# Kernel optimization log

Hardware: AMD Instinct MI355X
Metric: run time of the kernel (lower is better)

## Reference

```python
import jax, jax.numpy as jnp
import numpy as np

NUM_USER = 10000
NUM_ITEM = 30000
N = NUM_USER + NUM_ITEM          # total nodes
DIM = 64                          # dim_E == dim_C
E = 500000                        # user-item interactions
NUM_ROUTING = 3
ALPHA_THR = 0.5
NEG_SLOPE_ATTN = 0.2              # GAT attention leaky slope
NEG_SLOPE_ACT = 0.01              # F.leaky_relu_ default


def l2norm(x, eps=1e-12):
    n = jnp.linalg.norm(x, axis=-1, keepdims=True)
    return x / jnp.maximum(n, eps)


def seg_softmax(score, seg):
    # numerically-stable softmax over edges grouped by destination node
    m = jax.ops.segment_max(score, seg, num_segments=N)
    e = jnp.exp(score - m[seg])
    s = jax.ops.segment_sum(e, seg, num_segments=N)
    return e / (s[seg] + 1e-16)


def gat_ori(x, W, src, dst):
    # GATConv_ori: dot-product attention, softmax per destination, scatter-add
    h = x @ W                                     # [N, C]
    score = jax.nn.leaky_relu(jnp.sum(h[dst] * h[src], -1), NEG_SLOPE_ATTN)
    alpha = seg_softmax(score, dst)               # [2E]
    return jax.ops.segment_sum(alpha[:, None] * h[src], dst, num_segments=N)


def gat_pre(x, y, z, W, src, dst):
    # GATConv_pre: primary-modality attention modulated by cross-modal gate (reattn)
    hx = x @ W
    sx = jnp.sum(hx[dst] * hx[src], -1)
    sy = jnp.sum(y[dst] * y[src], -1)
    sz = jnp.sum(z[dst] * z[src], -1)
    alpha = seg_softmax(jax.nn.leaky_relu(sx, NEG_SLOPE_ATTN), dst)
    gate = jax.nn.sigmoid(0.5 * (sy + sz))
    alpha = jnp.where(gate > ALPHA_THR, alpha * gate, alpha)
    return jax.ops.segment_sum(alpha[:, None] * hx[src], dst, num_segments=N)


def cgcn(pref, feat, pref2, feat2, pref3, feat3, src, dst, Wpre, Wori):
    x = jnp.concatenate([pref, feat], 0)
    y = jnp.concatenate([pref2, feat2], 0)
    z = jnp.concatenate([pref3, feat3], 0)
    x = l2norm(gat_pre(x, y, z, Wpre, src, dst))
    for _ in range(NUM_ROUTING):
        x = l2norm(x + gat_ori(x, Wori, src, dst))
    return x


def gcn_conv(x, W, src, dst):
    return jax.ops.segment_sum((x @ W)[src], dst, num_segments=N)


def real_gcn(id_emb, Wg, src, dst):
    x = l2norm(id_emb)
    h1 = jax.nn.leaky_relu(gcn_conv(x, Wg[0], src, dst), NEG_SLOPE_ACT)
    h2 = jax.nn.leaky_relu(gcn_conv(h1, Wg[1], src, dst), NEG_SLOPE_ACT)
    h3 = gcn_conv(h1, Wg[2], src, dst)
    return x + h1 + h2 + h3


def setup_inputs() -> dict:
    key = jax.random.key(0)
    ks = jax.random.split(key, 16)
    users = jax.random.randint(ks[0], (E,), 0, NUM_USER)
    items = jax.random.randint(ks[1], (E,), NUM_USER, N)
    edge_index = jnp.stack([users, items]).astype(jnp.int64)
    s = 0.05
    return {
        'edge_index': edge_index,
        'v_feat': jax.random.normal(ks[2], (NUM_ITEM, 128), jnp.float32),
        'a_feat': jax.random.normal(ks[3], (NUM_ITEM, 128), jnp.float32),
        't_feat': jax.random.normal(ks[4], (NUM_ITEM, 100), jnp.float32),
        'pref_v': jax.random.normal(ks[5], (NUM_USER, DIM), jnp.float32) * s,
        'pref_a': jax.random.normal(ks[6], (NUM_USER, DIM), jnp.float32) * s,
        'pref_t': jax.random.normal(ks[7], (NUM_USER, DIM), jnp.float32) * s,
        'mlp_v_w': jax.random.normal(ks[8], (DIM, 128), jnp.float32) * s,
        'mlp_v_b': jnp.zeros((DIM,), jnp.float32),
        'mlp_a_w': jax.random.normal(ks[9], (DIM, 128), jnp.float32) * s,
        'mlp_a_b': jnp.zeros((DIM,), jnp.float32),
        'mlp_t_w': jax.random.normal(ks[10], (DIM, 100), jnp.float32) * s,
        'mlp_t_b': jnp.zeros((DIM,), jnp.float32),
        'pre_w': jax.random.normal(ks[11], (3, DIM, DIM), jnp.float32) * s,
        'ori_w': jax.random.normal(ks[12], (3, DIM, DIM), jnp.float32) * s,
        'gcn_w': jax.random.normal(ks[13], (3, DIM, DIM), jnp.float32) * s,
        'id_embedding': jax.random.normal(ks[14], (N, DIM), jnp.float32) * s,
    }


def reference(edge_index, v_feat, a_feat, t_feat, pref_v, pref_a, pref_t,
              mlp_v_w, mlp_v_b, mlp_a_w, mlp_a_b, mlp_t_w, mlp_t_b,
              pre_w, ori_w, gcn_w, id_embedding):
    # symmetrize edges (cat with flipped); no self-loops possible (bipartite)
    src = jnp.concatenate([edge_index[0], edge_index[1]])
    dst = jnp.concatenate([edge_index[1], edge_index[0]])

    fv = l2norm(jax.nn.leaky_relu(v_feat @ mlp_v_w.T + mlp_v_b, NEG_SLOPE_ACT))
    fa = l2norm(jax.nn.leaky_relu(a_feat @ mlp_a_w.T + mlp_a_b, NEG_SLOPE_ACT))
    ft = l2norm(jax.nn.leaky_relu(t_feat @ mlp_t_w.T + mlp_t_b, NEG_SLOPE_ACT))
    pv, pa, pt = l2norm(pref_v), l2norm(pref_a), l2norm(pref_t)

    v_rep = cgcn(pv, fv, pa, fa, pt, ft, src, dst, pre_w[0], ori_w[0])
    a_rep = cgcn(pa, fa, pv, fv, pt, ft, src, dst, pre_w[1], ori_w[1])
    t_rep = cgcn(pt, ft, pa, fa, pv, fv, src, dst, pre_w[2], ori_w[2])
    id_rep = real_gcn(id_embedding, gcn_w, src, dst)

    return jnp.concatenate([id_rep, v_rep, a_rep, t_rep], axis=1)  # [N, 4*DIM]
```

## Files before the change

### kernel.cpp

```cpp
#include <hip/hip_runtime.h>
#include <hip/hip_fp16.h>
#include <math.h>

#define NUSER 10000
#define NITEM 30000
#define NN    40000
#define DD    64
#define PLANE ((size_t)NN * DD)

typedef _Float16 hv2 __attribute__((ext_vector_type(2)));
typedef _Float16 half8v __attribute__((ext_vector_type(8)));
typedef float float4v __attribute__((ext_vector_type(4)));
union U2H { unsigned u; hv2 v; __half2 hh; };

#if defined(__has_builtin)
#if __has_builtin(__builtin_amdgcn_fdot2)
#define HAS_FDOT2 1
#endif
#endif

__device__ __forceinline__ float fdot2u(unsigned a, unsigned b, float c) {
#ifdef HAS_FDOT2
    U2H x, y;
    x.u = a;
    y.u = b;
    return __builtin_amdgcn_fdot2(x.v, y.v, c, false);
#else
    U2H x, y;
    x.u = a;
    y.u = b;
    float2 fa = __half22float2(x.hh), fb = __half22float2(y.hh);
    return c + fa.x * fb.x + fa.y * fb.y;
#endif
}

__device__ __forceinline__ float dot8(uint4 a, uint4 b) {
    float d = fdot2u(a.x, b.x, 0.f);
    d = fdot2u(a.y, b.y, d);
    d = fdot2u(a.z, b.z, d);
    d = fdot2u(a.w, b.w, d);
    return d;
}

__device__ __forceinline__ __half2 uh(unsigned u) { U2H x; x.u = u; return x.hh; }
__device__ __forceinline__ unsigned hu(__half2 h) { U2H x; x.hh = h; return x.u; }
__device__ __forceinline__ __half2 h2rx(__half2 v, int m) {
    return __hadd2(v, uh((unsigned)__shfl_xor((int)hu(v), m, 64)));
}

__device__ __forceinline__ float wsum(float v) {
#pragma unroll
    for (int o = 32; o > 0; o >>= 1) v += __shfl_xor(v, o, 64);
    return v;
}
__device__ __forceinline__ float qsum8(float v) {
    v += __shfl_xor(v, 1, 64);
    v += __shfl_xor(v, 2, 64);
    v += __shfl_xor(v, 4, 64);
    return v;
}
__device__ __forceinline__ float gsum8f(float v) {
    v += __shfl_xor(v, 8, 64);
    v += __shfl_xor(v, 16, 64);
    v += __shfl_xor(v, 32, 64);
    return v;
}

__device__ __forceinline__ int orderIF(int i) {
    return (i < NITEM) ? (NUSER + i) : (i - NITEM);
}

__global__ void k_hist(const int* ei, int E2, int E, int* cnt, int* posw) {
    int i = blockIdx.x * blockDim.x + threadIdx.x;
    if (i >= E2) return;
    int d = (i < E) ? ei[E + i] : ei[i - E];
    posw[i] = atomicAdd(&cnt[d], 1);
}

__global__ void k_bsum(const int* __restrict__ cnt, int* __restrict__ bsum, int n, int chunk) {
    __shared__ int wsh[4];
    int b = blockIdx.x, tid = threadIdx.x;
    int base = b * chunk, end = min(n, base + chunk);
    int s = 0;
    for (int i = base + tid; i < end; i += 256) s += cnt[i];
#pragma unroll
    for (int o = 32; o > 0; o >>= 1) s += __shfl_xor(s, o, 64);
    if ((tid & 63) == 0) wsh[tid >> 6] = s;
    __syncthreads();
    if (tid == 0) bsum[b] = wsh[0] + wsh[1] + wsh[2] + wsh[3];
}

__global__ void k_bscan(int* bsum, int nb, int* rp_end) {
    int lane = threadIdx.x;
    int v = (lane < nb) ? bsum[lane] : 0;
    int orig = v;
#pragma unroll
    for (int o = 1; o < 64; o <<= 1) {
        int y = __shfl_up(v, o, 64);
        if (lane >= o) v += y;
    }
    if (lane < nb) bsum[lane] = v - orig;
    if (lane == 63) *rp_end = v;
}

__global__ void k_apply(const int* __restrict__ cnt, const int* __restrict__ boff,
                        int* __restrict__ rp, int n, int chunk) {
    __shared__ int buf[256];
    __shared__ int csh;
    int b = blockIdx.x, tid = threadIdx.x;
    int base = b * chunk, end = min(n, base + chunk);
    int carry = boff[b];
    for (int t0 = base; t0 < end; t0 += 256) {
        int i = t0 + tid;
        int v = (i < end) ? cnt[i] : 0;
        int x = v;
        buf[tid] = x;
        __syncthreads();
        for (int o = 1; o < 256; o <<= 1) {
            int y = (tid >= o) ? buf[tid - o] : 0;
            __syncthreads();
            x += y;
            buf[tid] = x;
            __syncthreads();
        }
        if (i < end) rp[i] = carry + x - v;
        __syncthreads();
        if (tid == 255) csh = carry + x;
        __syncthreads();
        carry = csh;
    }
}

__global__ void k_scatter(const int* ei, int E2, int E, const int* rp,
                          const int* __restrict__ posw, int* col) {
    int i = blockIdx.x * blockDim.x + threadIdx.x;
    if (i >= E2) return;
    int j = (i < E) ? i : i - E;
    int s = (i < E) ? ei[j] : ei[E + j];
    int d = (i < E) ? ei[E + j] : ei[j];
    col[rp[d] + posw[i]] = s;
}

__global__ void k_prep_pref(const float* __restrict__ pv, const float* __restrict__ pa,
                            const float* __restrict__ pt, __half* __restrict__ M) {
    int t = blockIdx.x * blockDim.x + threadIdx.x;
    int w = t >> 6, lane = t & 63, nw = (gridDim.x * blockDim.x) >> 6;
    for (int r = w; r < NUSER; r += nw) {
        float a = pv[(size_t)r * DD + lane];
        float b = pa[(size_t)r * DD + lane];
        float c = pt[(size_t)r * DD + lane];
        float sa = a * a, sb = b * b, sc = c * c;
#pragma unroll
        for (int o = 32; o > 0; o >>= 1) {
            sa += __shfl_xor(sa, o, 64);
            sb += __shfl_xor(sb, o, 64);
            sc += __shfl_xor(sc, o, 64);
        }
        size_t base = (size_t)r * 3 * DD + lane;
        M[base] = __float2half(a / fmaxf(sqrtf(sa), 1e-12f));
        M[base + DD] = __float2half(b / fmaxf(sqrtf(sb), 1e-12f));
        M[base + 2 * DD] = __float2half(c / fmaxf(sqrtf(sc), 1e-12f));
    }
}

template <int K>
__global__ void k_mlp(const float* __restrict__ feat, const float* __restrict__ W,
                      const float* __restrict__ bias, __half* __restrict__ M, int mo) {
    constexpr int K4 = K / 4;
    __shared__ float4 Wl[K4][DD];
    __shared__ float4 rbuf[4][2][K4];
    int t = threadIdx.x, wib = t >> 6, lane = t & 63;
    for (int i = t; i < DD * K4; i += 256) {
        int c = i / K4, k4 = i - c * K4;
        Wl[k4][c] = *(const float4*)(W + (size_t)c * K + k4 * 4);
    }
    __syncthreads();
    float b = bias[lane];
    const int stride = gridDim.x * 4;
    int r = blockIdx.x * 4 + wib;
    float4 v = {0.f, 0.f, 0.f, 0.f};
    if (r < NITEM && lane < K4) v = *(const float4*)(feat + (size_t)r * K + lane * 4);
    int cur = 0;
    for (; r < NITEM; r += stride) {
        if (lane < K4) rbuf[wib][cur][lane] = v;
        int rn = r + stride;
        if (rn < NITEM && lane < K4) v = *(const float4*)(feat + (size_t)rn * K + lane * 4);
        asm volatile("s_waitcnt lgkmcnt(0)" ::: "memory");
        float acc = b;
#pragma unroll
        for (int k4 = 0; k4 < K4; k4++) {
            float4 x4 = rbuf[wib][cur][k4];
            float4 w4 = Wl[k4][lane];
            acc += x4.x * w4.x + x4.y * w4.y + x4.z * w4.z + x4.w * w4.w;
        }
        float h = acc > 0.f ? acc : 0.01f * acc;
        float n = sqrtf(wsum(h * h));
        M[((size_t)(NUSER + r) * 3 + mo) * DD + lane] = __float2half(h / fmaxf(n, 1e-12f));
        cur ^= 1;
    }
}

__global__ void k_gemm_mfma(const __half* __restrict__ x3, const float* __restrict__ W3,
                            __half* __restrict__ o3) {
    int mo = blockIdx.y;
    const float* W = W3 + (size_t)mo * 4096;
    int t = threadIdx.x, wv = t >> 6, lane = t & 63;
    int lr = lane & 15, lg = lane >> 4;
    half8v b[4][2];
#pragma unroll
    for (int ct = 0; ct < 4; ct++)
#pragma unroll
        for (int kh = 0; kh < 2; kh++)
#pragma unroll
            for (int i = 0; i < 8; i++)
                b[ct][kh][i] = (_Float16)W[(kh * 32 + lg * 8 + i) * 64 + ct * 16 + lr];
    const int NT = NN / 16;
    for (int rt = blockIdx.x * 4 + wv; rt < NT; rt += gridDim.x * 4) {
        const __half* xr = x3 + ((size_t)(rt * 16 + lr) * 3 + mo) * DD + lg * 8;
        half8v a0 = *(const half8v*)xr;
        half8v a1 = *(const half8v*)(xr + 32);
        float4v acc0 = {0.f, 0.f, 0.f, 0.f}, acc1 = acc0, acc2 = acc0, acc3 = acc0;
        acc0 = __builtin_amdgcn_mfma_f32_16x16x32_f16(a0, b[0][0], acc0, 0, 0, 0);
        acc1 = __builtin_amdgcn_mfma_f32_16x16x32_f16(a0, b[1][0], acc1, 0, 0, 0);
        acc2 = __builtin_amdgcn_mfma_f32_16x16x32_f16(a0, b[2][0], acc2, 0, 0, 0);
        acc3 = __builtin_amdgcn_mfma_f32_16x16x32_f16(a0, b[3][0], acc3, 0, 0, 0);
        acc0 = __builtin_amdgcn_mfma_f32_16x16x32_f16(a1, b[0][1], acc0, 0, 0, 0);
        acc1 = __builtin_amdgcn_mfma_f32_16x16x32_f16(a1, b[1][1], acc1, 0, 0, 0);
        acc2 = __builtin_amdgcn_mfma_f32_16x16x32_f16(a1, b[2][1], acc2, 0, 0, 0);
        acc3 = __builtin_amdgcn_mfma_f32_16x16x32_f16(a1, b[3][1], acc3, 0, 0, 0);
#pragma unroll
        for (int i = 0; i < 4; i++) {
            size_t rbase = ((size_t)(rt * 16 + lg * 4 + i) * 3 + mo) * DD + lr;
            o3[rbase] = __float2half(acc0[i]);
            o3[rbase + 16] = __float2half(acc1[i]);
            o3[rbase + 32] = __float2half(acc2[i]);
            o3[rbase + 48] = __float2half(acc3[i]);
        }
    }
}

__global__ void k_gemm_f2(const float* __restrict__ x, const float* __restrict__ W2,
                          __half* __restrict__ o2) {
    __shared__ float rowbuf[4][DD];
    int mo = blockIdx.y;
    const float* W = W2 + (size_t)mo * 4096;
    int t = threadIdx.x, wib = t >> 6, lane = t & 63;
    float Wc[DD];
#pragma unroll
    for (int k = 0; k < DD; k++) Wc[k] = W[k * DD + lane];
    for (int r = blockIdx.x * 4 + wib; r < NN; r += gridDim.x * 4) {
        rowbuf[wib][lane] = x[(size_t)r * DD + lane];
        asm volatile("s_waitcnt lgkmcnt(0)" ::: "memory");
        float acc = 0.f;
#pragma unroll
        for (int k4 = 0; k4 < DD / 4; k4++) {
            float4 xq = *(const float4*)&rowbuf[wib][k4 * 4];
            acc += xq.x * Wc[k4 * 4] + xq.y * Wc[k4 * 4 + 1] + xq.z * Wc[k4 * 4 + 2] +
                   xq.w * Wc[k4 * 4 + 3];
        }
        o2[((size_t)r * 2 + mo) * DD + lane] = __float2half(acc);
    }
}

__global__ void k_gemm_id(const float* __restrict__ x, const float* __restrict__ W,
                          __half* __restrict__ hout, float* __restrict__ xnorm) {
    __shared__ float rowbuf[4][DD];
    int t = threadIdx.x, wib = t >> 6, lane = t & 63;
    float Wc[DD];
#pragma unroll
    for (int k = 0; k < DD; k++) Wc[k] = W[k * DD + lane];
    for (int r = blockIdx.x * 4 + wib; r < NN; r += gridDim.x * 4) {
        float xv = x[(size_t)r * DD + lane];
        float n = sqrtf(wsum(xv * xv));
        xv /= fmaxf(n, 1e-12f);
        xnorm[(size_t)r * DD + lane] = xv;
        rowbuf[wib][lane] = xv;
        asm volatile("s_waitcnt lgkmcnt(0)" ::: "memory");
        float acc = 0.f;
#pragma unroll
        for (int k4 = 0; k4 < DD / 4; k4++) {
            float4 xq = *(const float4*)&rowbuf[wib][k4 * 4];
            acc += xq.x * Wc[k4 * 4] + xq.y * Wc[k4 * 4 + 1] + xq.z * Wc[k4 * 4 + 2] +
                   xq.w * Wc[k4 * 4 + 3];
        }
        hout[(size_t)r * DD + lane] = __float2half(acc);
    }
}

__device__ __forceinline__ float gatef(float ssum) {
    float gate = 1.f / (1.f + __expf(-0.5f * ssum));
    return gate > 0.5f ? gate : 1.f;
}

__global__ void k_gat_pre3(const __half* __restrict__ M, const __half* __restrict__ h3,
                           const int* __restrict__ rp, const int* __restrict__ col,
                           __half* __restrict__ x3h) {
    int t = blockIdx.x * blockDim.x + threadIdx.x;
    int wv = t >> 6, lane = t & 63, nw = (gridDim.x * blockDim.x) >> 6;
    int g = lane >> 3, q = lane & 7;
    const __half2 z = __floats2half2_rn(0.f, 0.f);
    for (int w0 = wv; w0 < NN; w0 += nw) {
        int n = orderIF(w0);
        int e0 = rp[n], e1 = rp[n + 1];
        const uint4* mrow = (const uint4*)(M + (size_t)n * 192);
        uint4 tv = mrow[q], ta = mrow[q + 8], tt = mrow[q + 16];
        const uint4* hrow = (const uint4*)(h3 + (size_t)n * 192);
        uint4 hd0 = hrow[q], hd1 = hrow[q + 8], hd2 = hrow[q + 16];
        float s0 = 0.f, s1 = 0.f, s2 = 0.f;
        __half2 a0[4] = {z, z, z, z}, a1[4] = {z, z, z, z}, a2[4] = {z, z, z, z};
        for (int eb = e0 + g; eb < e1; eb += 8) {
            int sn = col[eb];
            const uint4* srow = (const uint4*)(M + (size_t)sn * 192);
            uint4 sv = srow[q], sa = srow[q + 8], st = srow[q + 16];
            float dv = qsum8(dot8(tv, sv));
            float da = qsum8(dot8(ta, sa));
            float dt = qsum8(dot8(tt, st));
            float ga = gatef(da + dt), gb_ = gatef(dv + dt), gc = gatef(da + dv);
            const uint4* hsrow = (const uint4*)(h3 + (size_t)sn * 192);
            uint4 v0 = hsrow[q], v1 = hsrow[q + 8], v2 = hsrow[q + 16];
            float d0 = qsum8(dot8(hd0, v0));
            float d1 = qsum8(dot8(hd1, v1));
            float d2 = qsum8(dot8(hd2, v2));
            float sc0 = d0 > 0.f ? d0 : 0.2f * d0;
            float sc1 = d1 > 0.f ? d1 : 0.2f * d1;
            float sc2 = d2 > 0.f ? d2 : 0.2f * d2;
            float p0 = __expf(sc0), p1 = __expf(sc1), p2 = __expf(sc2);
            s0 += p0;
            s1 += p1;
            s2 += p2;
            __half2 ph0 = __float2half2_rn(p0 * ga);
            __half2 ph1 = __float2half2_rn(p1 * gb_);
            __half2 ph2 = __float2half2_rn(p2 * gc);
            a0[0] = __hfma2(ph0, uh(v0.x), a0[0]);
            a0[1] = __hfma2(ph0, uh(v0.y), a0[1]);
            a0[2] = __hfma2(ph0, uh(v0.z), a0[2]);
            a0[3] = __hfma2(ph0, uh(v0.w), a0[3]);
            a1[0] = __hfma2(ph1, uh(v1.x), a1[0]);
            a1[1] = __hfma2(ph1, uh(v1.y), a1[1]);
            a1[2] = __hfma2(ph1, uh(v1.z), a1[2]);
            a1[3] = __hfma2(ph1, uh(v1.w), a1[3]);
            a2[0] = __hfma2(ph2, uh(v2.x), a2[0]);
            a2[1] = __hfma2(ph2, uh(v2.y), a2[1]);
            a2[2] = __hfma2(ph2, uh(v2.z), a2[2]);
            a2[3] = __hfma2(ph2, uh(v2.w), a2[3]);
        }
        s0 = gsum8f(s0);
        s1 = gsum8f(s1);
        s2 = gsum8f(s2);
#pragma unroll
        for (int j = 0; j < 4; j++) {
            a0[j] = h2rx(h2rx(h2rx(a0[j], 8), 16), 32);
            a1[j] = h2rx(h2rx(h2rx(a1[j], 8), 16), 32);
            a2[j] = h2rx(h2rx(h2rx(a2[j], 8), 16), 32);
        }
        float i0 = 1.f / (s0 + 1e-16f), i1 = 1.f / (s1 + 1e-16f), i2 = 1.f / (s2 + 1e-16f);
        float o0[8], o1[8], o2[8];
#pragma unroll
        for (int j = 0; j < 4; j++) {
            float2 f0 = __half22float2(a0[j]);
            float2 f1 = __half22float2(a1[j]);
            float2 f2 = __half22float2(a2[j]);
            o0[2 * j] = f0.x * i0;
            o0[2 * j + 1] = f0.y * i0;
            o1[2 * j] = f1.x * i1;
            o1[2 * j + 1] = f1.y * i1;
            o2[2 * j] = f2.x * i2;
            o2[2 * j + 1] = f2.y * i2;
        }
        float n0 = 0.f, n1 = 0.f, n2 = 0.f;
#pragma unroll
        for (int k = 0; k < 8; k++) {
            n0 += o0[k] * o0[k];
            n1 += o1[k] * o1[k];
            n2 += o2[k] * o2[k];
        }
        n0 = qsum8(n0);
        n1 = qsum8(n1);
        n2 = qsum8(n2);
        float r0 = 1.f / fmaxf(sqrtf(n0), 1e-12f);
        float r1 = 1.f / fmaxf(sqrtf(n1), 1e-12f);
        float r2 = 1.f / fmaxf(sqrtf(n2), 1e-12f);
        if (g == 0) {
            uint4* orow = (uint4*)(x3h + (size_t)n * 192);
            uint4 w0_, w1_, w2_;
            w0_.x = hu(__floats2half2_rn(o0[0] * r0, o0[1] * r0));
            w0_.y = hu(__floats2half2_rn(o0[2] * r0, o0[3] * r0));
            w0_.z = hu(__floats2half2_rn(o0[4] * r0, o0[5] * r0));
            w0_.w = hu(__floats2half2_rn(o0[6] * r0, o0[7] * r0));
            w1_.x = hu(__floats2half2_rn(o1[0] * r1, o1[1] * r1));
            w1_.y = hu(__floats2half2_rn(o1[2] * r1, o1[3] * r1));
            w1_.z = hu(__floats2half2_rn(o1[4] * r1, o1[5] * r1));
            w1_.w = hu(__floats2half2_rn(o1[6] * r1, o1[7] * r1));
            w2_.x = hu(__floats2half2_rn(o2[0] * r2, o2[1] * r2));
            w2_.y = hu(__floats2half2_rn(o2[2] * r2, o2[3] * r2));
            w2_.z = hu(__floats2half2_rn(o2[4] * r2, o2[5] * r2));
            w2_.w = hu(__floats2half2_rn(o2[6] * r2, o2[7] * r2));
            orow[q] = w0_;
            orow[q + 8] = w1_;
            orow[q + 16] = w2_;
        }
    }
}

__global__ void k_gat_ori3(const __half* __restrict__ h3, const __half* __restrict__ x3h,
                           const int* __restrict__ rp, const int* __restrict__ col,
                           __half* __restrict__ xout, float* __restrict__ fout) {
    int t = blockIdx.x * blockDim.x + threadIdx.x;
    int wv = t >> 6, lane = t & 63, nw = (gridDim.x * blockDim.x) >> 6;
    int g = lane >> 3, q = lane & 7;
    const __half2 z = __floats2half2_rn(0.f, 0.f);
    for (int w0 = wv; w0 < NN; w0 += nw) {
        int n = orderIF(w0);
        int e0 = rp[n], e1 = rp[n + 1];
        const uint4* hrow = (const uint4*)(h3 + (size_t)n * 192);
        uint4 hd0 = hrow[q], hd1 = hrow[q + 8], hd2 = hrow[q + 16];
        float s0 = 0.f, s1 = 0.f, s2 = 0.f;
        __half2 a0[4] = {z, z, z, z}, a1[4] = {z, z, z, z}, a2[4] = {z, z, z, z};
        for (int eb = e0 + g; eb < e1; eb += 8) {
            int sn = col[eb];
            const uint4* srow = (const uint4*)(h3 + (size_t)sn * 192);
            uint4 v0 = srow[q], v1 = srow[q + 8], v2 = srow[q + 16];
            float d0 = qsum8(dot8(hd0, v0));
            float d1 = qsum8(dot8(hd1, v1));
            float d2 = qsum8(dot8(hd2, v2));
            float sc0 = d0 > 0.f ? d0 : 0.2f * d0;
            float sc1 = d1 > 0.f ? d1 : 0.2f * d1;
            float sc2 = d2 > 0.f ? d2 : 0.2f * d2;
            float p0 = __expf(sc0), p1 = __expf(sc1), p2 = __expf(sc2);
            s0 += p0;
            s1 += p1;
            s2 += p2;
            __half2 ph0 = __float2half2_rn(p0);
            __half2 ph1 = __float2half2_rn(p1);
            __half2 ph2 = __float2half2_rn(p2);
            a0[0] = __hfma2(ph0, uh(v0.x), a0[0]);
            a0[1] = __hfma2(ph0, uh(v0.y), a0[1]);
            a0[2] = __hfma2(ph0, uh(v0.z), a0[2]);
            a0[3] = __hfma2(ph0, uh(v0.w), a0[3]);
            a1[0] = __hfma2(ph1, uh(v1.x), a1[0]);
            a1[1] = __hfma2(ph1, uh(v1.y), a1[1]);
            a1[2] = __hfma2(ph1, uh(v1.z), a1[2]);
            a1[3] = __hfma2(ph1, uh(v1.w), a1[3]);
            a2[0] = __hfma2(ph2, uh(v2.x), a2[0]);
            a2[1] = __hfma2(ph2, uh(v2.y), a2[1]);
            a2[2] = __hfma2(ph2, uh(v2.z), a2[2]);
            a2[3] = __hfma2(ph2, uh(v2.w), a2[3]);
        }
        s0 = gsum8f(s0);
        s1 = gsum8f(s1);
        s2 = gsum8f(s2);
#pragma unroll
        for (int j = 0; j < 4; j++) {
            a0[j] = h2rx(h2rx(h2rx(a0[j], 8), 16), 32);
            a1[j] = h2rx(h2rx(h2rx(a1[j], 8), 16), 32);
            a2[j] = h2rx(h2rx(h2rx(a2[j], 8), 16), 32);
        }
        float i0 = 1.f / (s0 + 1e-16f), i1 = 1.f / (s1 + 1e-16f), i2 = 1.f / (s2 + 1e-16f);
        const uint4* xrow = (const uint4*)(x3h + (size_t)n * 192);
        uint4 xr0 = xrow[q], xr1 = xrow[q + 8], xr2 = xrow[q + 16];
        float o0[8], o1[8], o2[8];
#pragma unroll
        for (int j = 0; j < 4; j++) {
            float2 f0 = __half22float2(a0[j]);
            float2 f1 = __half22float2(a1[j]);
            float2 f2 = __half22float2(a2[j]);
            float2 xf0 = __half22float2(uh(j == 0 ? xr0.x : j == 1 ? xr0.y : j == 2 ? xr0.z : xr0.w));
            float2 xf1 = __half22float2(uh(j == 0 ? xr1.x : j == 1 ? xr1.y : j == 2 ? xr1.z : xr1.w));
            float2 xf2 = __half22float2(uh(j == 0 ? xr2.x : j == 1 ? xr2.y : j == 2 ? xr2.z : xr2.w));
            o0[2 * j] = xf0.x + f0.x * i0;
            o0[2 * j + 1] = xf0.y + f0.y * i0;
            o1[2 * j] = xf1.x + f1.x * i1;
            o1[2 * j + 1] = xf1.y + f1.y * i1;
            o2[2 * j] = xf2.x + f2.x * i2;
            o2[2 * j + 1] = xf2.y + f2.y * i2;
        }
        float n0 = 0.f, n1 = 0.f, n2 = 0.f;
#pragma unroll
        for (int k = 0; k < 8; k++) {
            n0 += o0[k] * o0[k];
            n1 += o1[k] * o1[k];
            n2 += o2[k] * o2[k];
        }
        n0 = qsum8(n0);
        n1 = qsum8(n1);
        n2 = qsum8(n2);
        float r0 = 1.f / fmaxf(sqrtf(n0), 1e-12f);
        float r1 = 1.f / fmaxf(sqrtf(n1), 1e-12f);
        float r2 = 1.f / fmaxf(sqrtf(n2), 1e-12f);
        if (g == 0) {
            if (fout) {
                float* ob = fout + (size_t)n * 256 + 64 + q * 8;
                *(float4*)(ob) = make_float4(o0[0] * r0, o0[1] * r0, o0[2] * r0, o0[3] * r0);
                *(float4*)(ob + 4) = make_float4(o0[4] * r0, o0[5] * r0, o0[6] * r0, o0[7] * r0);
                *(float4*)(ob + 64) = make_float4(o1[0] * r1, o1[1] * r1, o1[2] * r1, o1[3] * r1);
                *(float4*)(ob + 68) = make_float4(o1[4] * r1, o1[5] * r1, o1[6] * r1, o1[7] * r1);
                *(float4*)(ob + 128) = make_float4(o2[0] * r2, o2[1] * r2, o2[2] * r2, o2[3] * r2);
                *(float4*)(ob + 132) = make_float4(o2[4] * r2, o2[5] * r2, o2[6] * r2, o2[7] * r2);
            } else {
                uint4* orow = (uint4*)(xout + (size_t)n * 192);
                uint4 w0_, w1_, w2_;
                w0_.x = hu(__floats2half2_rn(o0[0] * r0, o0[1] * r0));
                w0_.y = hu(__floats2half2_rn(o0[2] * r0, o0[3] * r0));
                w0_.z = hu(__floats2half2_rn(o0[4] * r0, o0[5] * r0));
                w0_.w = hu(__floats2half2_rn(o0[6] * r0, o0[7] * r0));
                w1_.x = hu(__floats2half2_rn(o1[0] * r1, o1[1] * r1));
                w1_.y = hu(__floats2half2_rn(o1[2] * r1, o1[3] * r1));
                w1_.z = hu(__floats2half2_rn(o1[4] * r1, o1[5] * r1));
                w1_.w = hu(__floats2half2_rn(o1[6] * r1, o1[7] * r1));
                w2_.x = hu(__floats2half2_rn(o2[0] * r2, o2[1] * r2));
                w2_.y = hu(__floats2half2_rn(o2[2] * r2, o2[3] * r2));
                w2_.z = hu(__floats2half2_rn(o2[4] * r2, o2[5] * r2));
                w2_.w = hu(__floats2half2_rn(o2[6] * r2, o2[7] * r2));
                orow[q] = w0_;
                orow[q + 8] = w1_;
                orow[q + 16] = w2_;
            }
        }
    }
}

__global__ void k_gcn1(const __half* __restrict__ h, const int* __restrict__ rp,
                       const int* __restrict__ col, float* __restrict__ out) {
    int t = blockIdx.x * blockDim.x + threadIdx.x;
    int wv = t >> 6, lane = t & 63, nw = (gridDim.x * blockDim.x) >> 6;
    int g = lane >> 3, q = lane & 7;
    const __half2 z = __floats2half2_rn(0.f, 0.f);
    for (int w0 = wv; w0 < NN; w0 += nw) {
        int n = orderIF(w0);
        int e0 = rp[n], e1 = rp[n + 1];
        __half2 a[4] = {z, z, z, z};
        for (int eb = e0 + g; eb < e1; eb += 8) {
            int sn = col[eb];
            uint4 v = ((const uint4*)(h + (size_t)sn * DD))[q];
            a[0] = __hadd2(a[0], uh(v.x));
            a[1] = __hadd2(a[1], uh(v.y));
            a[2] = __hadd2(a[2], uh(v.z));
            a[3] = __hadd2(a[3], uh(v.w));
        }
#pragma unroll
        for (int j = 0; j < 4; j++) a[j] = h2rx(h2rx(h2rx(a[j], 8), 16), 32);
        if (g == 0) {
            float o[8];
#pragma unroll
            for (int j = 0; j < 4; j++) {
                float2 f = __half22float2(a[j]);
                o[2 * j] = f.x > 0.f ? f.x : 0.01f * f.x;
                o[2 * j + 1] = f.y > 0.f ? f.y : 0.01f * f.y;
            }
            float* ob = out + (size_t)n * DD + q * 8;
            *(float4*)(ob) = make_float4(o[0], o[1], o[2], o[3]);
            *(float4*)(ob + 4) = make_float4(o[4], o[5], o[6], o[7]);
        }
    }
}

__global__ void k_gcn_final2(const __half* __restrict__ gp, const int* __restrict__ rp,
                             const int* __restrict__ col, const float* __restrict__ x0,
                             const float* __restrict__ h1, float* __restrict__ out) {
    int t = blockIdx.x * blockDim.x + threadIdx.x;
    int wv = t >> 6, lane = t & 63, nw = (gridDim.x * blockDim.x) >> 6;
    int g = lane >> 3, q = lane & 7;
    const __half2 z = __floats2half2_rn(0.f, 0.f);
    for (int w0 = wv; w0 < NN; w0 += nw) {
        int n = orderIF(w0);
        int e0 = rp[n], e1 = rp[n + 1];
        __half2 aA[4] = {z, z, z, z}, aB[4] = {z, z, z, z};
        for (int eb = e0 + g; eb < e1; eb += 8) {
            int sn = col[eb];
            const uint4* base = (const uint4*)(gp + (size_t)sn * 128);
            uint4 vA = base[q], vB = base[q + 8];
            aA[0] = __hadd2(aA[0], uh(vA.x));
            aA[1] = __hadd2(aA[1], uh(vA.y));
            aA[2] = __hadd2(aA[2], uh(vA.z));
            aA[3] = __hadd2(aA[3], uh(vA.w));
            aB[0] = __hadd2(aB[0], uh(vB.x));
            aB[1] = __hadd2(aB[1], uh(vB.y));
            aB[2] = __hadd2(aB[2], uh(vB.z));
            aB[3] = __hadd2(aB[3], uh(vB.w));
        }
#pragma unroll
        for (int j = 0; j < 4; j++) {
            aA[j] = h2rx(h2rx(h2rx(aA[j], 8), 16), 32);
            aB[j] = h2rx(h2rx(h2rx(aB[j], 8), 16), 32);
        }
        if (g == 0) {
            const float* p0 = x0 + (size_t)n * DD + q * 8;
            const float* p1 = h1 + (size_t)n * DD + q * 8;
            float4 v0a = *(const float4*)(p0), v0b = *(const float4*)(p0 + 4);
            float4 v1a = *(const float4*)(p1), v1b = *(const float4*)(p1 + 4);
            float o[8];
#pragma unroll
            for (int j = 0; j < 4; j++) {
                float2 fA = __half22float2(aA[j]);
                float2 fB = __half22float2(aB[j]);
                float h2x = fA.x > 0.f ? fA.x : 0.01f * fA.x;
                float h2y = fA.y > 0.f ? fA.y : 0.01f * fA.y;
                o[2 * j] = h2x + fB.x;
                o[2 * j + 1] = h2y + fB.y;
            }
            float* ob = out + (size_t)n * 256 + q * 8;
            *(float4*)(ob) = make_float4(o[0] + v0a.x + v1a.x, o[1] + v0a.y + v1a.y,
                                         o[2] + v0a.z + v1a.z, o[3] + v0a.w + v1a.w);
            *(float4*)(ob + 4) = make_float4(o[4] + v0b.x + v1b.x, o[5] + v0b.y + v1b.y,
                                             o[6] + v0b.z + v1b.z, o[7] + v0b.w + v1b.w);
        }
    }
}

extern "C" void kernel_launch(void* const* d_in, const int* in_sizes, int n_in,
                              void* d_out, int out_size, void* d_ws, size_t ws_size,
                              hipStream_t stream) {
    const int* ei       = (const int*)d_in[0];
    const float* v_feat = (const float*)d_in[1];
    const float* a_feat = (const float*)d_in[2];
    const float* t_feat = (const float*)d_in[3];
    const float* pref_v = (const float*)d_in[4];
    const float* pref_a = (const float*)d_in[5];
    const float* pref_t = (const float*)d_in[6];
    const float* mlp_v_w = (const float*)d_in[7];
    const float* mlp_v_b = (const float*)d_in[8];
    const float* mlp_a_w = (const float*)d_in[9];
    const float* mlp_a_b = (const float*)d_in[10];
    const float* mlp_t_w = (const float*)d_in[11];
    const float* mlp_t_b = (const float*)d_in[12];
    const float* pre_w  = (const float*)d_in[13];
    const float* ori_w  = (const float*)d_in[14];
    const float* gcn_w  = (const float*)d_in[15];
    const float* id_emb = (const float*)d_in[16];
    float* out = (float*)d_out;

    const int E2 = in_sizes[0];
    const int E  = E2 / 2;

    char* w = (char*)d_ws;
    auto alloc = [&](size_t bytes) -> void* {
        void* p = (void*)w;
        w += (bytes + 255) & ~(size_t)255;
        return p;
    };
    int* cnt  = (int*)alloc((size_t)NN * 4);
    int* rp   = (int*)alloc((size_t)(NN + 1) * 4);
    int* bsum = (int*)alloc(256);
    int* col  = (int*)alloc((size_t)E2 * 4);
    int* posw = (int*)alloc((size_t)E2 * 4);
    __half* Mh3  = (__half*)alloc(3 * PLANE * 2);
    __half* hb3h = (__half*)alloc(3 * PLANE * 2);
    __half* x3h  = (__half*)alloc(3 * PLANE * 2);
    float* x0f = (float*)alloc(PLANE * 4);
    float* h1f = (float*)alloc(PLANE * 4);

    __half* g1 = hb3h;
    __half* gpair = hb3h + PLANE;

    const int NBLK = 64, CHUNK = (NN + NBLK - 1) / NBLK;
    hipMemsetAsync(cnt, 0, (size_t)NN * 4, stream);
    k_hist<<<(E2 + 255) / 256, 256, 0, stream>>>(ei, E2, E, cnt, posw);
    k_bsum<<<NBLK, 256, 0, stream>>>(cnt, bsum, NN, CHUNK);
    k_bscan<<<1, 64, 0, stream>>>(bsum, NBLK, rp + NN);
    k_apply<<<NBLK, 256, 0, stream>>>(cnt, bsum, rp, NN, CHUNK);
    k_scatter<<<(E2 + 255) / 256, 256, 0, stream>>>(ei, E2, E, rp, posw, col);

    k_prep_pref<<<640, 256, 0, stream>>>(pref_v, pref_a, pref_t, Mh3);
    k_mlp<128><<<1024, 256, 0, stream>>>(v_feat, mlp_v_w, mlp_v_b, Mh3, 0);
    k_mlp<128><<<1024, 256, 0, stream>>>(a_feat, mlp_a_w, mlp_a_b, Mh3, 1);
    k_mlp<100><<<1024, 256, 0, stream>>>(t_feat, mlp_t_w, mlp_t_b, Mh3, 2);

    const int GB = (NN + 3) / 4;

    dim3 gm(640, 3);
    k_gemm_mfma<<<gm, 256, 0, stream>>>(Mh3, pre_w, hb3h);
    k_gat_pre3<<<GB, 256, 0, stream>>>(Mh3, hb3h, rp, col, x3h);
    for (int it = 0; it < 3; it++) {
        k_gemm_mfma<<<gm, 256, 0, stream>>>(x3h, ori_w, hb3h);
        if (it < 2)
            k_gat_ori3<<<GB, 256, 0, stream>>>(hb3h, x3h, rp, col, x3h, nullptr);
        else
            k_gat_ori3<<<GB, 256, 0, stream>>>(hb3h, x3h, rp, col, nullptr, out);
    }

    k_gemm_id<<<1280, 256, 0, stream>>>(id_emb, gcn_w, g1, x0f);
    k_gcn1<<<GB, 256, 0, stream>>>(g1, rp, col, h1f);
    dim3 g2(1280, 2);
    k_gemm_f2<<<g2, 256, 0, stream>>>(h1f, gcn_w + 4096, gpair);
    k_gcn_final2<<<GB, 256, 0, stream>>>(gpair, rp, col, x0f, h1f, out);
}
```

Baseline: 546.5 us.

## Fuse GCN neighbor aggregations into the GAT pre and final ori passes

The id-GCN branch's two edge-gather passes (k_gcn1 and k_gcn_final2) are folded into the existing GAT kernels. The first GCN aggregation now runs inside k_gat_pre3 and the second inside a new final-iteration k_gat_ori3f, so the CSR traversal and col reads are shared and two launches go away. To allow this, g1 and gpair get their own buffers instead of aliasing hb3h, and the GCN GEMMs are moved earlier in the schedule. The fused kernels carry more live registers and more gather traffic per edge, which may lower occupancy.

```diff
diff --git a/kernel.cpp b/kernel.cpp
--- a/kernel.cpp
+++ b/kernel.cpp
@@ -293,8 +293,9 @@
 }
 
 __global__ void k_gat_pre3(const __half* __restrict__ M, const __half* __restrict__ h3,
-                           const int* __restrict__ rp, const int* __restrict__ col,
-                           __half* __restrict__ x3h) {
+                           const __half* __restrict__ g1, const int* __restrict__ rp,
+                           const int* __restrict__ col, __half* __restrict__ x3h,
+                           float* __restrict__ h1f) {
     int t = blockIdx.x * blockDim.x + threadIdx.x;
     int wv = t >> 6, lane = t & 63, nw = (gridDim.x * blockDim.x) >> 6;
     int g = lane >> 3, q = lane & 7;
@@ -308,6 +309,7 @@
         uint4 hd0 = hrow[q], hd1 = hrow[q + 8], hd2 = hrow[q + 16];
         float s0 = 0.f, s1 = 0.f, s2 = 0.f;
         __half2 a0[4] = {z, z, z, z}, a1[4] = {z, z, z, z}, a2[4] = {z, z, z, z};
+        __half2 ag[4] = {z, z, z, z};
         for (int eb = e0 + g; eb < e1; eb += 8) {
             int sn = col[eb];
             const uint4* srow = (const uint4*)(M + (size_t)sn * 192);
@@ -318,6 +320,7 @@
             float ga = gatef(da + dt), gb_ = gatef(dv + dt), gc = gatef(da + dv);
             const uint4* hsrow = (const uint4*)(h3 + (size_t)sn * 192);
             uint4 v0 = hsrow[q], v1 = hsrow[q + 8], v2 = hsrow[q + 16];
+            uint4 vg = ((const uint4*)(g1 + (size_t)sn * DD))[q];
             float d0 = qsum8(dot8(hd0, v0));
             float d1 = qsum8(dot8(hd1, v1));
             float d2 = qsum8(dot8(hd2, v2));
@@ -343,6 +346,10 @@
             a2[1] = __hfma2(ph2, uh(v2.y), a2[1]);
             a2[2] = __hfma2(ph2, uh(v2.z), a2[2]);
             a2[3] = __hfma2(ph2, uh(v2.w), a2[3]);
+            ag[0] = __hadd2(ag[0], uh(vg.x));
+            ag[1] = __hadd2(ag[1], uh(vg.y));
+            ag[2] = __hadd2(ag[2], uh(vg.z));
+            ag[3] = __hadd2(ag[3], uh(vg.w));
         }
         s0 = gsum8f(s0);
         s1 = gsum8f(s1);
@@ -352,6 +359,7 @@
             a0[j] = h2rx(h2rx(h2rx(a0[j], 8), 16), 32);
             a1[j] = h2rx(h2rx(h2rx(a1[j], 8), 16), 32);
             a2[j] = h2rx(h2rx(h2rx(a2[j], 8), 16), 32);
+            ag[j] = h2rx(h2rx(h2rx(ag[j], 8), 16), 32);
         }
         float i0 = 1.f / (s0 + 1e-16f), i1 = 1.f / (s1 + 1e-16f), i2 = 1.f / (s2 + 1e-16f);
         float o0[8], o1[8], o2[8];
@@ -398,13 +406,23 @@
             orow[q] = w0_;
             orow[q + 8] = w1_;
             orow[q + 16] = w2_;
+            float og[8];
+#pragma unroll
+            for (int j = 0; j < 4; j++) {
+                float2 f = __half22float2(ag[j]);
+                og[2 * j] = f.x > 0.f ? f.x : 0.01f * f.x;
+                og[2 * j + 1] = f.y > 0.f ? f.y : 0.01f * f.y;
+            }
+            float* ob = h1f + (size_t)n * DD + q * 8;
+            *(float4*)(ob) = make_float4(og[0], og[1], og[2], og[3]);
+            *(float4*)(ob + 4) = make_float4(og[4], og[5], og[6], og[7]);
         }
     }
 }
 
 __global__ void k_gat_ori3(const __half* __restrict__ h3, const __half* __restrict__ x3h,
                            const int* __restrict__ rp, const int* __restrict__ col,
-                           __half* __restrict__ xout, float* __restrict__ fout) {
+                           __half* __restrict__ xout) {
     int t = blockIdx.x * blockDim.x + threadIdx.x;
     int wv = t >> 6, lane = t & 63, nw = (gridDim.x * blockDim.x) >> 6;
     int g = lane >> 3, q = lane & 7;
@@ -488,39 +506,31 @@
         float r1 = 1.f / fmaxf(sqrtf(n1), 1e-12f);
         float r2 = 1.f / fmaxf(sqrtf(n2), 1e-12f);
         if (g == 0) {
-            if (fout) {
-                float* ob = fout + (size_t)n * 256 + 64 + q * 8;
-                *(float4*)(ob) = make_float4(o0[0] * r0, o0[1] * r0, o0[2] * r0, o0[3] * r0);
-                *(float4*)(ob + 4) = make_float4(o0[4] * r0, o0[5] * r0, o0[6] * r0, o0[7] * r0);
-                *(float4*)(ob + 64) = make_float4(o1[0] * r1, o1[1] * r1, o1[2] * r1, o1[3] * r1);
-                *(float4*)(ob + 68) = make_float4(o1[4] * r1, o1[5] * r1, o1[6] * r1, o1[7] * r1);
-                *(float4*)(ob + 128) = make_float4(o2[0] * r2, o2[1] * r2, o2[2] * r2, o2[3] * r2);
-                *(float4*)(ob + 132) = make_float4(o2[4] * r2, o2[5] * r2, o2[6] * r2, o2[7] * r2);
-            } else {
-                uint4* orow = (uint4*)(xout + (size_t)n * 192);
-                uint4 w0_, w1_, w2_;
-                w0_.x = hu(__floats2half2_rn(o0[0] * r0, o0[1] * r0));
-                w0_.y = hu(__floats2half2_rn(o0[2] * r0, o0[3] * r0));
-                w0_.z = hu(__floats2half2_rn(o0[4] * r0, o0[5] * r0));
-                w0_.w = hu(__floats2half2_rn(o0[6] * r0, o0[7] * r0));
-                w1_.x = hu(__floats2half2_rn(o1[0] * r1, o1[1] * r1));
-                w1_.y = hu(__floats2half2_rn(o1[2] * r1, o1[3] * r1));
-                w1_.z = hu(__floats2half2_rn(o1[4] * r1, o1[5] * r1));
-                w1_.w = hu(__floats2half2_rn(o1[6] * r1, o1[7] * r1));
-                w2_.x = hu(__floats2half2_rn(o2[0] * r2, o2[1] * r2));
-                w2_.y = hu(__floats2half2_rn(o2[2] * r2, o2[3] * r2));
-                w2_.z = hu(__floats2half2_rn(o2[4] * r2, o2[5] * r2));
-                w2_.w = hu(__floats2half2_rn(o2[6] * r2, o2[7] * r2));
-                orow[q] = w0_;
-                orow[q + 8] = w1_;
-                orow[q + 16] = w2_;
-            }
-        }
-    }
-}
-
-__global__ void k_gcn1(const __half* __restrict__ h, const int* __restrict__ rp,
-                       const int* __restrict__ col, float* __restrict__ out) {
+            uint4* orow = (uint4*)(xout + (size_t)n * 192);
+            uint4 w0_, w1_, w2_;
+            w0_.x = hu(__floats2half2_rn(o0[0] * r0, o0[1] * r0));
+            w0_.y = hu(__floats2half2_rn(o0[2] * r0, o0[3] * r0));
+            w0_.z = hu(__floats2half2_rn(o0[4] * r0, o0[5] * r0));
+            w0_.w = hu(__floats2half2_rn(o0[6] * r0, o0[7] * r0));
+            w1_.x = hu(__floats2half2_rn(o1[0] * r1, o1[1] * r1));
+            w1_.y = hu(__floats2half2_rn(o1[2] * r1, o1[3] * r1));
+            w1_.z = hu(__floats2half2_rn(o1[4] * r1, o1[5] * r1));
+            w1_.w = hu(__floats2half2_rn(o1[6] * r1, o1[7] * r1));
+            w2_.x = hu(__floats2half2_rn(o2[0] * r2, o2[1] * r2));
+            w2_.y = hu(__floats2half2_rn(o2[2] * r2, o2[3] * r2));
+            w2_.z = hu(__floats2half2_rn(o2[4] * r2, o2[5] * r2));
+            w2_.w = hu(__floats2half2_rn(o2[6] * r2, o2[7] * r2));
+            orow[q] = w0_;
+            orow[q + 8] = w1_;
+            orow[q + 16] = w2_;
+        }
+    }
+}
+
+__global__ void k_gat_ori3f(const __half* __restrict__ h3, const __half* __restrict__ x3h,
+                            const __half* __restrict__ gp, const float* __restrict__ x0,
+                            const float* __restrict__ h1, const int* __restrict__ rp,
+                            const int* __restrict__ col, float* __restrict__ out) {
     int t = blockIdx.x * blockDim.x + threadIdx.x;
     int wv = t >> 6, lane = t & 63, nw = (gridDim.x * blockDim.x) >> 6;
     int g = lane >> 3, q = lane & 7;
@@ -528,47 +538,42 @@
     for (int w0 = wv; w0 < NN; w0 += nw) {
         int n = orderIF(w0);
         int e0 = rp[n], e1 = rp[n + 1];
-        __half2 a[4] = {z, z, z, z};
-        for (int eb = e0 + g; eb < e1; eb += 8) {
-            int sn = col[eb];
-            uint4 v = ((const uint4*)(h + (size_t)sn * DD))[q];
-            a[0] = __hadd2(a[0], uh(v.x));
-            a[1] = __hadd2(a[1], uh(v.y));
-            a[2] = __hadd2(a[2], uh(v.z));
-            a[3] = __hadd2(a[3], uh(v.w));
-        }
-#pragma unroll
-        for (int j = 0; j < 4; j++) a[j] = h2rx(h2rx(h2rx(a[j], 8), 16), 32);
-        if (g == 0) {
-            float o[8];
-#pragma unroll
-            for (int j = 0; j < 4; j++) {
-                float2 f = __half22float2(a[j]);
-                o[2 * j] = f.x > 0.f ? f.x : 0.01f * f.x;
-                o[2 * j + 1] = f.y > 0.f ? f.y : 0.01f * f.y;
-            }
-            float* ob = out + (size_t)n * DD + q * 8;
-            *(float4*)(ob) = make_float4(o[0], o[1], o[2], o[3]);
-            *(float4*)(ob + 4) = make_float4(o[4], o[5], o[6], o[7]);
-        }
-    }
-}
-
-__global__ void k_gcn_final2(const __half* __restrict__ gp, const int* __restrict__ rp,
-                             const int* __restrict__ col, const float* __restrict__ x0,
-                             const float* __restrict__ h1, float* __restrict__ out) {
-    int t = blockIdx.x * blockDim.x + threadIdx.x;
-    int wv = t >> 6, lane = t & 63, nw = (gridDim.x * blockDim.x) >> 6;
-    int g = lane >> 3, q = lane & 7;
-    const __half2 z = __floats2half2_rn(0.f, 0.f);
-    for (int w0 = wv; w0 < NN; w0 += nw) {
-        int n = orderIF(w0);
-        int e0 = rp[n], e1 = rp[n + 1];
+        const uint4* hrow = (const uint4*)(h3 + (size_t)n * 192);
+        uint4 hd0 = hrow[q], hd1 = hrow[q + 8], hd2 = hrow[q + 16];
+        float s0 = 0.f, s1 = 0.f, s2 = 0.f;
+        __half2 a0[4] = {z, z, z, z}, a1[4] = {z, z, z, z}, a2[4] = {z, z, z, z};
         __half2 aA[4] = {z, z, z, z}, aB[4] = {z, z, z, z};
         for (int eb = e0 + g; eb < e1; eb += 8) {
             int sn = col[eb];
-            const uint4* base = (const uint4*)(gp + (size_t)sn * 128);
-            uint4 vA = base[q], vB = base[q + 8];
+            const uint4* srow = (const uint4*)(h3 + (size_t)sn * 192);
+            uint4 v0 = srow[q], v1 = srow[q + 8], v2 = srow[q + 16];
+            const uint4* gbase = (const uint4*)(gp + (size_t)sn * 128);
+            uint4 vA = gbase[q], vB = gbase[q + 8];
+            float d0 = qsum8(dot8(hd0, v0));
+            float d1 = qsum8(dot8(hd1, v1));
+            float d2 = qsum8(dot8(hd2, v2));
+            float sc0 = d0 > 0.f ? d0 : 0.2f * d0;
+            float sc1 = d1 > 0.f ? d1 : 0.2f * d1;
+            float sc2 = d2 > 0.f ? d2 : 0.2f * d2;
+            float p0 = __expf(sc0), p1 = __expf(sc1), p2 = __expf(sc2);
+            s0 += p0;
+            s1 += p1;
+            s2 += p2;
+            __half2 ph0 = __float2half2_rn(p0);
+            __half2 ph1 = __float2half2_rn(p1);
+            __half2 ph2 = __float2half2_rn(p2);
+            a0[0] = __hfma2(ph0, uh(v0.x), a0[0]);
+            a0[1] = __hfma2(ph0, uh(v0.y), a0[1]);
+            a0[2] = __hfma2(ph0, uh(v0.z), a0[2]);
+            a0[3] = __hfma2(ph0, uh(v0.w), a0[3]);
+            a1[0] = __hfma2(ph1, uh(v1.x), a1[0]);
+            a1[1] = __hfma2(ph1, uh(v1.y), a1[1]);
+            a1[2] = __hfma2(ph1, uh(v1.z), a1[2]);
+            a1[3] = __hfma2(ph1, uh(v1.w), a1[3]);
+            a2[0] = __hfma2(ph2, uh(v2.x), a2[0]);
+            a2[1] = __hfma2(ph2, uh(v2.y), a2[1]);
+            a2[2] = __hfma2(ph2, uh(v2.z), a2[2]);
+            a2[3] = __hfma2(ph2, uh(v2.w), a2[3]);
             aA[0] = __hadd2(aA[0], uh(vA.x));
             aA[1] = __hadd2(aA[1], uh(vA.y));
             aA[2] = __hadd2(aA[2], uh(vA.z));
@@ -578,31 +583,75 @@
             aB[2] = __hadd2(aB[2], uh(vB.z));
             aB[3] = __hadd2(aB[3], uh(vB.w));
         }
+        s0 = gsum8f(s0);
+        s1 = gsum8f(s1);
+        s2 = gsum8f(s2);
 #pragma unroll
         for (int j = 0; j < 4; j++) {
+            a0[j] = h2rx(h2rx(h2rx(a0[j], 8), 16), 32);
+            a1[j] = h2rx(h2rx(h2rx(a1[j], 8), 16), 32);
+            a2[j] = h2rx(h2rx(h2rx(a2[j], 8), 16), 32);
             aA[j] = h2rx(h2rx(h2rx(aA[j], 8), 16), 32);
             aB[j] = h2rx(h2rx(h2rx(aB[j], 8), 16), 32);
         }
+        float i0 = 1.f / (s0 + 1e-16f), i1 = 1.f / (s1 + 1e-16f), i2 = 1.f / (s2 + 1e-16f);
+        const uint4* xrow = (const uint4*)(x3h + (size_t)n * 192);
+        uint4 xr0 = xrow[q], xr1 = xrow[q + 8], xr2 = xrow[q + 16];
+        float o0[8], o1[8], o2[8];
+#pragma unroll
+        for (int j = 0; j < 4; j++) {
+            float2 f0 = __half22float2(a0[j]);
+            float2 f1 = __half22float2(a1[j]);
+            float2 f2 = __half22float2(a2[j]);
+            float2 xf0 = __half22float2(uh(j == 0 ? xr0.x : j == 1 ? xr0.y : j == 2 ? xr0.z : xr0.w));
+            float2 xf1 = __half22float2(uh(j == 0 ? xr1.x : j == 1 ? xr1.y : j == 2 ? xr1.z : xr1.w));
+            float2 xf2 = __half22float2(uh(j == 0 ? xr2.x : j == 1 ? xr2.y : j == 2 ? xr2.z : xr2.w));
+            o0[2 * j] = xf0.x + f0.x * i0;
+            o0[2 * j + 1] = xf0.y + f0.y * i0;
+            o1[2 * j] = xf1.x + f1.x * i1;
+            o1[2 * j + 1] = xf1.y + f1.y * i1;
+            o2[2 * j] = xf2.x + f2.x * i2;
+            o2[2 * j + 1] = xf2.y + f2.y * i2;
+        }
+        float n0 = 0.f, n1 = 0.f, n2 = 0.f;
+#pragma unroll
+        for (int k = 0; k < 8; k++) {
+            n0 += o0[k] * o0[k];
+            n1 += o1[k] * o1[k];
+            n2 += o2[k] * o2[k];
+        }
+        n0 = qsum8(n0);
+        n1 = qsum8(n1);
+        n2 = qsum8(n2);
+        float r0 = 1.f / fmaxf(sqrtf(n0), 1e-12f);
+        float r1 = 1.f / fmaxf(sqrtf(n1), 1e-12f);
+        float r2 = 1.f / fmaxf(sqrtf(n2), 1e-12f);
         if (g == 0) {
+            float* ob = out + (size_t)n * 256 + q * 8;
             const float* p0 = x0 + (size_t)n * DD + q * 8;
             const float* p1 = h1 + (size_t)n * DD + q * 8;
             float4 v0a = *(const float4*)(p0), v0b = *(const float4*)(p0 + 4);
             float4 v1a = *(const float4*)(p1), v1b = *(const float4*)(p1 + 4);
-            float o[8];
+            float og[8];
 #pragma unroll
             for (int j = 0; j < 4; j++) {
                 float2 fA = __half22float2(aA[j]);
                 float2 fB = __half22float2(aB[j]);
-                float h2x = fA.x > 0.f ? fA.x : 0.01f * fA.x;
-                float h2y = fA.y > 0.f ? fA.y : 0.01f * fA.y;
-                o[2 * j] = h2x + fB.x;
-                o[2 * j + 1] = h2y + fB.y;
+                float hx = fA.x > 0.f ? fA.x : 0.01f * fA.x;
+                float hy = fA.y > 0.f ? fA.y : 0.01f * fA.y;
+                og[2 * j] = hx + fB.x;
+                og[2 * j + 1] = hy + fB.y;
             }
-            float* ob = out + (size_t)n * 256 + q * 8;
-            *(float4*)(ob) = make_float4(o[0] + v0a.x + v1a.x, o[1] + v0a.y + v1a.y,
-                                         o[2] + v0a.z + v1a.z, o[3] + v0a.w + v1a.w);
-            *(float4*)(ob + 4) = make_float4(o[4] + v0b.x + v1b.x, o[5] + v0b.y + v1b.y,
-                                             o[6] + v0b.z + v1b.z, o[7] + v0b.w + v1b.w);
+            *(float4*)(ob) = make_float4(og[0] + v0a.x + v1a.x, og[1] + v0a.y + v1a.y,
+                                         og[2] + v0a.z + v1a.z, og[3] + v0a.w + v1a.w);
+            *(float4*)(ob + 4) = make_float4(og[4] + v0b.x + v1b.x, og[5] + v0b.y + v1b.y,
+                                             og[6] + v0b.z + v1b.z, og[7] + v0b.w + v1b.w);
+            *(float4*)(ob + 64) = make_float4(o0[0] * r0, o0[1] * r0, o0[2] * r0, o0[3] * r0);
+            *(float4*)(ob + 68) = make_float4(o0[4] * r0, o0[5] * r0, o0[6] * r0, o0[7] * r0);
+            *(float4*)(ob + 128) = make_float4(o1[0] * r1, o1[1] * r1, o1[2] * r1, o1[3] * r1);
+            *(float4*)(ob + 132) = make_float4(o1[4] * r1, o1[5] * r1, o1[6] * r1, o1[7] * r1);
+            *(float4*)(ob + 192) = make_float4(o2[0] * r2, o2[1] * r2, o2[2] * r2, o2[3] * r2);
+            *(float4*)(ob + 196) = make_float4(o2[4] * r2, o2[5] * r2, o2[6] * r2, o2[7] * r2);
         }
     }
 }
@@ -646,11 +695,10 @@
     __half* Mh3  = (__half*)alloc(3 * PLANE * 2);
     __half* hb3h = (__half*)alloc(3 * PLANE * 2);
     __half* x3h  = (__half*)alloc(3 * PLANE * 2);
+    __half* g1   = (__half*)alloc(PLANE * 2);
+    __half* gpair = (__half*)alloc(2 * PLANE * 2);
     float* x0f = (float*)alloc(PLANE * 4);
     float* h1f = (float*)alloc(PLANE * 4);
-
-    __half* g1 = hb3h;
-    __half* gpair = hb3h + PLANE;
 
     const int NBLK = 64, CHUNK = (NN + NBLK - 1) / NBLK;
     hipMemsetAsync(cnt, 0, (size_t)NN * 4, stream);
@@ -667,20 +715,20 @@
 
     const int GB = (NN + 3) / 4;
 
+    k_gemm_id<<<1280, 256, 0, stream>>>(id_emb, gcn_w, g1, x0f);
+
     dim3 gm(640, 3);
     k_gemm_mfma<<<gm, 256, 0, stream>>>(Mh3, pre_w, hb3h);
-    k_gat_pre3<<<GB, 256, 0, stream>>>(Mh3, hb3h, rp, col, x3h);
+    k_gat_pre3<<<GB, 256, 0, stream>>>(Mh3, hb3h, g1, rp, col, x3h, h1f);
+
+    dim3 g2(1280, 2);
+    k_gemm_f2<<<g2, 256, 0, stream>>>(h1f, gcn_w + 4096, gpair);
+
     for (int it = 0; it < 3; it++) {
         k_gemm_mfma<<<gm, 256, 0, stream>>>(x3h, ori_w, hb3h);
         if (it < 2)
-            k_gat_ori3<<<GB, 256, 0, stream>>>(hb3h, x3h, rp, col, x3h, nullptr);
+            k_gat_ori3<<<GB, 256, 0, stream>>>(hb3h, x3h, rp, col, x3h);
         else
-            k_gat_ori3<<<GB, 256, 0, stream>>>(hb3h, x3h, rp, col, nullptr, out);
-    }
-
-    k_gemm_id<<<1280, 256, 0, stream>>>(id_emb, gcn_w, g1, x0f);
-    k_gcn1<<<GB, 256, 0, stream>>>(g1, rp, col, h1f);
-    dim3 g2(1280, 2);
-    k_gemm_f2<<<g2, 256, 0, stream>>>(h1f, gcn_w + 4096, gpair);
-    k_gcn_final2<<<GB, 256, 0, stream>>>(gpair, rp, col, x0f, h1f, out);
-}
+            k_gat_ori3f<<<GB, 256, 0, stream>>>(hb3h, x3h, gpair, x0f, h1f, rp, col, out);
+    }
+}
```

After: 542.9 us. No clear change (-0.6%).
